# Kernel tuning notes

Hardware: AMD Instinct MI355X
Metric: run time of the kernel (lower is better)

## Reference

```python
import jax, jax.numpy as jnp
import numpy as np

B, C, L = 32, 512, 16          # batch, clauses per CNF, max literals per clause
D, H, P = 256, 1024, 16        # clause_hidden_dim, hidden_size, prefix_tokens
NH, NL = 8, 4                  # adapter_heads, adapter_layers
MAXV = 512                     # max_variables


def _ln(x, w, b, eps=1e-5):
    m = jnp.mean(x, axis=-1, keepdims=True)
    v = jnp.mean(jnp.square(x - m), axis=-1, keepdims=True)
    return (x - m) * jax.lax.rsqrt(v + eps) * w + b


def _mha(q, k, v, w_in, b_in, w_out, b_out, nh):
    E = q.shape[-1]
    dh = E // nh
    wq, wk, wv = jnp.split(w_in, 3, axis=0)
    bq, bk, bv = jnp.split(b_in, 3, axis=0)

    def heads(x, w, b):
        y = x @ w.T + b
        return y.reshape(x.shape[0], x.shape[1], nh, dh).transpose(0, 2, 1, 3)

    qh, kh, vh = heads(q, wq, bq), heads(k, wk, bk), heads(v, wv, bv)
    att = jax.nn.softmax(jnp.einsum('bhqd,bhkd->bhqk', qh, kh) * (1.0 / np.sqrt(dh)), axis=-1)
    o = jnp.einsum('bhqk,bhkd->bhqd', att, vh).transpose(0, 2, 1, 3).reshape(q.shape[0], q.shape[1], E)
    return o @ w_out.T + b_out


def setup_inputs() -> dict:
    key = jax.random.key(0)
    ks = jax.random.split(key, 16)
    s = 0.02
    var_idx = jax.random.randint(ks[0], (B, C, L), 0, MAXV + 1)
    sign_idx = jax.random.randint(ks[1], (B, C, L), 1, 3)   # 1=positive literal, 2=negative
    lens = jax.random.randint(ks[2], (B, C), 1, L + 1)      # ragged clause lengths >= 1
    lit_mask = jnp.arange(L)[None, None, :] < lens[..., None]
    inp = dict(var_idx=var_idx, sign_idx=sign_idx, lit_mask=lit_mask)
    inp['var_emb'] = jax.random.normal(ks[3], (MAXV + 1, D)) * s
    inp['sign_emb'] = jax.random.normal(ks[4], (3, D)) * s
    inp['litpos_emb'] = jax.random.normal(ks[5], (L, D)) * s
    inp['clausepos_emb'] = jax.random.normal(ks[6], (C, D)) * s
    inp['enc_in_w'] = jax.random.normal(ks[7], (NL, 3 * D, D)) * s
    inp['enc_in_b'] = jnp.zeros((NL, 3 * D))
    inp['enc_out_w'] = jax.random.normal(ks[8], (NL, D, D)) * s
    inp['enc_out_b'] = jnp.zeros((NL, D))
    inp['enc_ff1_w'] = jax.random.normal(ks[9], (NL, 4 * D, D)) * s
    inp['enc_ff1_b'] = jnp.zeros((NL, 4 * D))
    inp['enc_ff2_w'] = jax.random.normal(ks[10], (NL, D, 4 * D)) * s
    inp['enc_ff2_b'] = jnp.zeros((NL, D))
    inp['enc_n1_w'] = jnp.ones((NL, D))
    inp['enc_n1_b'] = jnp.zeros((NL, D))
    inp['enc_n2_w'] = jnp.ones((NL, D))
    inp['enc_n2_b'] = jnp.zeros((NL, D))
    inp['th_ln_w'] = jnp.ones((D,))
    inp['th_ln_b'] = jnp.zeros((D,))
    inp['th_w'] = jax.random.normal(ks[11], (H, D)) * s
    inp['th_b'] = jnp.zeros((H,))
    inp['pq'] = jax.random.normal(ks[12], (P, H))
    inp['pa_in_w'] = jax.random.normal(ks[13], (3 * H, H)) * s
    inp['pa_in_b'] = jnp.zeros((3 * H,))
    inp['pa_out_w'] = jax.random.normal(ks[14], (H, H)) * s
    inp['pa_out_b'] = jnp.zeros((H,))
    inp['pn_w'] = jnp.ones((H,))
    inp['pn_b'] = jnp.zeros((H,))
    return inp


def reference(var_idx, sign_idx, lit_mask, var_emb, sign_emb, litpos_emb, clausepos_emb,
              enc_in_w, enc_in_b, enc_out_w, enc_out_b, enc_ff1_w, enc_ff1_b,
              enc_ff2_w, enc_ff2_b, enc_n1_w, enc_n1_b, enc_n2_w, enc_n2_b,
              th_ln_w, th_ln_b, th_w, th_b, pq, pa_in_w, pa_in_b, pa_out_w, pa_out_b,
              pn_w, pn_b):
    # literal states [B,C,L,D]: four embedding gathers fused into one expression
    lit = (var_emb[var_idx] + sign_emb[sign_idx]
           + litpos_emb[None, None, :, :] + clausepos_emb[None, :, None, :])
    m = lit_mask[..., None].astype(lit.dtype)
    x = jnp.sum(lit * m, axis=2) / jnp.sum(m, axis=2)   # masked mean-pool -> [B,C,D]
    for i in range(NL):  # PyTorch post-norm TransformerEncoderLayer, gelu (exact)
        a = _mha(x, x, x, enc_in_w[i], enc_in_b[i], enc_out_w[i], enc_out_b[i], NH)
        x = _ln(x + a, enc_n1_w[i], enc_n1_b[i])
        f = jax.nn.gelu(x @ enc_ff1_w[i].T + enc_ff1_b[i], approximate=False) @ enc_ff2_w[i].T + enc_ff2_b[i]
        x = _ln(x + f, enc_n2_w[i], enc_n2_b[i])
    ch = _ln(x, th_ln_w, th_ln_b) @ th_w.T + th_b       # to_hidden -> [B,C,H]
    q = jnp.broadcast_to(pq[None], (ch.shape[0], P, H))
    pref = _mha(q, ch, ch, pa_in_w, pa_in_b, pa_out_w, pa_out_b, NH)
    return _ln(pref + q, pn_w, pn_b)                    # [B,P,H]
```

## Files before the change

kernel.cpp:

```cpp
#include <hip/hip_runtime.h>
#include <hip/hip_bf16.h>

typedef unsigned short u16;
typedef unsigned int u32;
typedef __attribute__((ext_vector_type(8))) short short8;
typedef __attribute__((ext_vector_type(4))) float floatx4;

#define BB 32
#define CC 512
#define LL 16
#define DD 256
#define HH 1024
#define PP 16
#define NLAY 4

__device__ __forceinline__ float bf2f(u16 u) {
  u32 x = ((u32)u) << 16; float f; __builtin_memcpy(&f, &x, 4); return f;
}
__device__ __forceinline__ u16 f2bf(float f) {
  __hip_bfloat16 h = __float2bfloat16(f);
  u16 r; __builtin_memcpy(&r, &h, 2); return r;
}
__device__ __forceinline__ void gload_lds16(const u16* g, u16* l) {
  __builtin_amdgcn_global_load_lds(
// ... 156 lines not shown
  }
  u32 cv = *(const u32*)&cpeb[c * DD + dl];
  float inv = 1.f / (float)cnt;
  u32 pk = (u32)f2bf(a0 * inv + bf2f((u16)cv)) | ((u32)f2bf(a1 * inv + bf2f((u16)(cv >> 16))) << 16);
  *(u32*)&xb[(size_t)bc * DD + dl] = pk;
}

template<int NC, bool GELU, bool LN, bool DLN>
__global__ __launch_bounds__(256) void gwide_kernel(
    const u16* __restrict__ A, const u16* __restrict__ W, const float* __restrict__ bias,
    const u16* __restrict__ resb, const float* __restrict__ gam, const float* __restrict__ bet,
    const float* __restrict__ gam2, const float* __restrict__ bet2,
    u16* __restrict__ out, int N, int K)
{
  constexpr int NT = NC / 32;
  constexpr int NT4 = NC / 64;
  __shared__ __align__(16) u16 As[32 * 64];
  __shared__ __align__(16) u16 Ws[NC * 64];
  __shared__ float sred[32][4][2];
  __shared__ float sred2[32][4][2];
  int t = threadIdx.x, lane = t & 63, w = t >> 6;
  int mrow = lane & 15, quad = lane >> 4;
  int bn0 = blockIdx.x * NC, bm0 = blockIdx.y * 32;

  int rA = t >> 3, gcA = (t & 7) ^ (rA & 7);
  const u16* gAp = A + (size_t)(bm0 + rA) * K + gcA * 8;
  u16* lAp = As + (w * 64) * 8;
  const u16* gW0 = W + (size_t)(bn0 + rA) * K + gcA * 8;
  u16* lW0 = Ws + (w * 64) * 8;

  floatx4 acc[2][NT4];
  #pragma unroll
  for (int mi = 0; mi < 2; ++mi)
    #pragma unroll
    for (int nt = 0; nt < NT4; ++nt) acc[mi][nt] = (floatx4){0.f, 0.f, 0.f, 0.f};

  for (int k0 = 0; k0 < K; k0 += 64) {
    __syncthreads();
    gload_lds16(gAp, lAp); gAp += 64;
    #pragma unroll
    for (int i = 0; i < NT; ++i)
      gload_lds16(gW0 + (size_t)i * 32 * K, lW0 + i * 2048);
    gW0 += 64;
    __syncthreads();
    #pragma unroll
    for (int ks = 0; ks < 2; ++ks) {
      int sw = ((ks * 4 + quad) ^ (mrow & 7)) * 8;
      short8 af0 = *(const short8*)&As[mrow * 64 + sw];
      short8 af1 = *(const short8*)&As[(16 + mrow) * 64 + sw];
      #pragma unroll
      for (int nt = 0; nt < NT4; ++nt) {
        int rw = w * (NC / 4) + nt * 16 + mrow;
        short8 bf = *(const short8*)&Ws[rw * 64 + sw];
        acc[0][nt] = __builtin_amdgcn_mfma_f32_16x16x32_bf16(af0, bf, acc[0][nt], 0, 0, 0);
        acc[1][nt] = __builtin_amdgcn_mfma_f32_16x16x32_bf16(af1, bf, acc[1][nt], 0, 0, 0);
      }
    }
  }

  if constexpr (LN) {
    float val[2][NT4][4];
    float bv[NT4];
    #pragma unroll
    for (int nt = 0; nt < NT4; ++nt) bv[nt] = bias[w * 64 + nt * 16 + mrow];
    #pragma unroll
    for (int mi = 0; mi < 2; ++mi) {
      #pragma unroll
      for (int r = 0; r < 4; ++r) {
        int gm = bm0 + mi * 16 + quad * 4 + r;
        float sr = 0.f, s2r = 0.f;
        #pragma unroll
        for (int nt = 0; nt < NT4; ++nt) {
          int gn = w * 64 + nt * 16 + mrow;
          float v = acc[mi][nt][r] + bv[nt] + bf2f(resb[(size_t)gm * 256 + gn]);
          val[mi][nt][r] = v; sr += v; s2r += v * v;
        }
        sr += __shfl_xor(sr, 1); s2r += __shfl_xor(s2r, 1);
        sr += __shfl_xor(sr, 2); s2r += __shfl_xor(s2r, 2);
        sr += __shfl_xor(sr, 4); s2r += __shfl_xor(s2r, 4);
        sr += __shfl_xor(sr, 8); s2r += __shfl_xor(s2r, 8);
        if (mrow == 0) { sred[mi * 16 + quad * 4 + r][w][0] = sr; sred[mi * 16 + quad * 4 + r][w][1] = s2r; }
      }
    }
    __syncthreads();
    #pragma unroll
    for (int mi = 0; mi < 2; ++mi) {
      #pragma unroll
      for (int r = 0; r < 4; ++r) {
        int lrow = mi * 16 + quad * 4 + r;
        float S  = sred[lrow][0][0] + sred[lrow][1][0] + sred[lrow][2][0] + sred[lrow][3][0];
        float S2 = sred[lrow][0][1] + sred[lrow][1][1] + sred[lrow][2][1] + sred[lrow][3][1];
        float mean = S * (1.f / 256.f);
        float var = S2 * (1.f / 256.f) - mean * mean;
        float inv = rsqrtf(var + 1e-5f);
        float sr2 = 0.f, s2r2 = 0.f;
        #pragma unroll
        for (int nt = 0; nt < NT4; ++nt) {
          int gn = w * 64 + nt * 16 + mrow;
          float y = (val[mi][nt][r] - mean) * inv * gam[gn] + bet[gn];
          val[mi][nt][r] = y;
          if constexpr (DLN) { sr2 += y; s2r2 += y * y; }
          else out[(size_t)(bm0 + lrow) * 256 + gn] = f2bf(y);
        }
        if constexpr (DLN) {
          sr2 += __shfl_xor(sr2, 1); s2r2 += __shfl_xor(s2r2, 1);
          sr2 += __shfl_xor(sr2, 2); s2r2 += __shfl_xor(s2r2, 2);
          sr2 += __shfl_xor(sr2, 4); s2r2 += __shfl_xor(s2r2, 4);
          sr2 += __shfl_xor(sr2, 8); s2r2 += __shfl_xor(s2r2, 8);
          if (mrow == 0) { sred2[lrow][w][0] = sr2; sred2[lrow][w][1] = s2r2; }
        }
      }
    }
    if constexpr (DLN) {
      __syncthreads();
      #pragma unroll
      for (int mi = 0; mi < 2; ++mi) {
        #pragma unroll
        for (int r = 0; r < 4; ++r) {
          int lrow = mi * 16 + quad * 4 + r;
          float S  = sred2[lrow][0][0] + sred2[lrow][1][0] + sred2[lrow][2][0] + sred2[lrow][3][0];
          float S2 = sred2[lrow][0][1] + sred2[lrow][1][1] + sred2[lrow][2][1] + sred2[lrow][3][1];
          float mean = S * (1.f / 256.f);
          float var = S2 * (1.f / 256.f) - mean * mean;
          float inv = rsqrtf(var + 1e-5f);
          #pragma unroll
          for (int nt = 0; nt < NT4; ++nt) {
            int gn = w * 64 + nt * 16 + mrow;
            float z = (val[mi][nt][r] - mean) * inv * gam2[gn] + bet2[gn];
            out[(size_t)(bm0 + lrow) * 256 + gn] = f2bf(z);
          }
        }
      }
    }
  } else {
    #pragma unroll
    for (int nt = 0; nt < NT4; ++nt) {
      int gn = bn0 + w * (NC / 4) + nt * 16 + mrow;
      float bv = bias[gn];
      #pragma unroll
      for (int mi = 0; mi < 2; ++mi) {
        #pragma unroll
        for (int r = 0; r < 4; ++r) {
          int gm = bm0 + mi * 16 + quad * 4 + r;
          float v = acc[mi][nt][r] + bv;
          if (GELU) v = 0.5f * v * (1.f + erff(v * 0.70710678118654752f));
          out[(size_t)gm * N + gn] = f2bf(v);
        }
      }
    }
  }
}

template<bool DLN>
__global__ __launch_bounds__(256) void ffu_kernel(
    const u16* __restrict__ A, const u16* __restrict__ W1, const float* __restrict__ b1,
    const u16* __restrict__ W2, const float* __restrict__ b2,
    const u16* __restrict__ resb,
    const float* __restrict__ gam, const float* __restrict__ bet,
    const float* __restrict__ gam2, const float* __restrict__ bet2,
    u16* __restrict__ out)
{
  __shared__ __align__(16) u16 As[2048];
  __shared__ __align__(16) u16 Ws[8 * 2048];
  __shared__ __align__(16) u16 Hs[4 * 2048];
  int t = threadIdx.x, lane = t & 63, w = t >> 6;
  int mrow = lane & 15, quad = lane >> 4;
  int bm0 = blockIdx.x * 32;
  int rA = t >> 3, gcA = (t & 7) ^ (rA & 7);

  floatx4 yacc[2][4];
  #pragma unroll
  for (int mi = 0; mi < 2; ++mi)
    #pragma unroll
    for (int nt = 0; nt < 4; ++nt) yacc[mi][nt] = (floatx4){0.f, 0.f, 0.f, 0.f};

  for (int nq = 0; nq < 4; ++nq) {
    floatx4 hacc[2][4];
    #pragma unroll
    for (int mi = 0; mi < 2; ++mi)
      #pragma unroll
      for (int nt = 0; nt < 4; ++nt) hacc[mi][nt] = (floatx4){0.f, 0.f, 0.f, 0.f};
    for (int kt = 0; kt < 4; ++kt) {
      __syncthreads();
      gload_lds16(A + (size_t)(bm0 + rA) * 256 + kt * 64 + gcA * 8, As + (w * 64) * 8);
      #pragma unroll
      for (int i = 0; i < 8; ++i)
        gload_lds16(W1 + (size_t)(nq * 256 + i * 32 + rA) * 256 + kt * 64 + gcA * 8,
                    Ws + i * 2048 + (w * 64) * 8);
      __syncthreads();
      #pragma unroll
      for (int ks = 0; ks < 2; ++ks) {
        int sw = ((ks * 4 + quad) ^ (mrow & 7)) * 8;
        short8 af0 = *(const short8*)&As[mrow * 64 + sw];
        short8 af1 = *(const short8*)&As[(16 + mrow) * 64 + sw];
        #pragma unroll
        for (int nt = 0; nt < 4; ++nt) {
          short8 bf = *(const short8*)&Ws[(w * 64 + nt * 16 + mrow) * 64 + sw];
          hacc[0][nt] = __builtin_amdgcn_mfma_f32_16x16x32_bf16(af0, bf, hacc[0][nt], 0, 0, 0);
          hacc[1][nt] = __builtin_amdgcn_mfma_f32_16x16x32_bf16(af1, bf, hacc[1][nt], 0, 0, 0);
        }
      }
    }
    {
      float bv1[4];
      #pragma unroll
      for (int nt = 0; nt < 4; ++nt) bv1[nt] = b1[nq * 256 + w * 64 + nt * 16 + mrow];
      #pragma unroll
      for (int mi = 0; mi < 2; ++mi) {
        #pragma unroll
        for (int nt = 0; nt < 4; ++nt) {
          int g = nt * 2 + (mrow >> 3);
          #pragma unroll
          for (int r = 0; r < 4; ++r) {
            int row = mi * 16 + quad * 4 + r;
            float v = hacc[mi][nt][r] + bv1[nt];
            v = 0.5f * v * (1.f + erff(v * 0.70710678118654752f));
            Hs[w * 2048 + row * 64 + (g ^ (row & 7)) * 8 + (mrow & 7)] = f2bf(v);
          }
        }
      }
    }
    for (int kt2 = 0; kt2 < 4; ++kt2) {
      __syncthreads();
      #pragma unroll
      for (int i = 0; i < 8; ++i)
        gload_lds16(W2 + (size_t)(i * 32 + rA) * 1024 + nq * 256 + kt2 * 64 + gcA * 8,
                    Ws + i * 2048 + (w * 64) * 8);
      __syncthreads();
      #pragma unroll
      for (int ks = 0; ks < 2; ++ks) {
        int sw = ((ks * 4 + quad) ^ (mrow & 7)) * 8;
        short8 af0 = *(const short8*)&Hs[kt2 * 2048 + mrow * 64 + sw];
        short8 af1 = *(const short8*)&Hs[kt2 * 2048 + (16 + mrow) * 64 + sw];
        #pragma unroll
        for (int nt = 0; nt < 4; ++nt) {
          short8 bf = *(const short8*)&Ws[(w * 64 + nt * 16 + mrow) * 64 + sw];
          yacc[0][nt] = __builtin_amdgcn_mfma_f32_16x16x32_bf16(af0, bf, yacc[0][nt], 0, 0, 0);
          yacc[1][nt] = __builtin_amdgcn_mfma_f32_16x16x32_bf16(af1, bf, yacc[1][nt], 0, 0, 0);
        }
      }
    }
  }
  __syncthreads();
  float* sred  = (float*)Hs;
  float* sred2 = (float*)(Hs + 2048);
  float val[2][4][4];
  float bv[4];
  #pragma unroll
  for (int nt = 0; nt < 4; ++nt) bv[nt] = b2[w * 64 + nt * 16 + mrow];
  #pragma unroll
  for (int mi = 0; mi < 2; ++mi) {
    #pragma unroll
    for (int r = 0; r < 4; ++r) {
      int gm = bm0 + mi * 16 + quad * 4 + r;
      float sr = 0.f, s2r = 0.f;
      #pragma unroll
      for (int nt = 0; nt < 4; ++nt) {
        int gn = w * 64 + nt * 16 + mrow;
        float v = yacc[mi][nt][r] + bv[nt] + bf2f(resb[(size_t)gm * 256 + gn]);
        val[mi][nt][r] = v; sr += v; s2r += v * v;
      }
      sr += __shfl_xor(sr, 1); s2r += __shfl_xor(s2r, 1);
      sr += __shfl_xor(sr, 2); s2r += __shfl_xor(s2r, 2);
      sr += __shfl_xor(sr, 4); s2r += __shfl_xor(s2r, 4);
      sr += __shfl_xor(sr, 8); s2r += __shfl_xor(s2r, 8);
      if (mrow == 0) {
        int lrow = mi * 16 + quad * 4 + r;
        sred[lrow * 8 + w * 2 + 0] = sr; sred[lrow * 8 + w * 2 + 1] = s2r;
      }
    }
  }
  __syncthreads();
  #pragma unroll
  for (int mi = 0; mi < 2; ++mi) {
    #pragma unroll
    for (int r = 0; r < 4; ++r) {
      int lrow = mi * 16 + quad * 4 + r;
      float S  = sred[lrow * 8 + 0] + sred[lrow * 8 + 2] + sred[lrow * 8 + 4] + sred[lrow * 8 + 6];
      float S2 = sred[lrow * 8 + 1] + sred[lrow * 8 + 3] + sred[lrow * 8 + 5] + sred[lrow * 8 + 7];
      float mean = S * (1.f / 256.f);
      float var = S2 * (1.f / 256.f) - mean * mean;
      float inv = rsqrtf(var + 1e-5f);
      float sr2 = 0.f, s2r2 = 0.f;
      #pragma unroll
      for (int nt = 0; nt < 4; ++nt) {
        int gn = w * 64 + nt * 16 + mrow;
        float y = (val[mi][nt][r] - mean) * inv * gam[gn] + bet[gn];
        val[mi][nt][r] = y;
        if constexpr (DLN) { sr2 += y; s2r2 += y * y; }
        else out[(size_t)(bm0 + lrow) * 256 + gn] = f2bf(y);
      }
      if constexpr (DLN) {
        sr2 += __shfl_xor(sr2, 1); s2r2 += __shfl_xor(s2r2, 1);
        sr2 += __shfl_xor(sr2, 2); s2r2 += __shfl_xor(s2r2, 2);
        sr2 += __shfl_xor(sr2, 4); s2r2 += __shfl_xor(s2r2, 4);
        sr2 += __shfl_xor(sr2, 8); s2r2 += __shfl_xor(s2r2, 8);
        if (mrow == 0) {
          sred2[lrow * 8 + w * 2 + 0] = sr2; sred2[lrow * 8 + w * 2 + 1] = s2r2;
        }
      }
    }
  }
  if constexpr (DLN) {
    __syncthreads();
    #pragma unroll
    for (int mi = 0; mi < 2; ++mi) {
      #pragma unroll
      for (int r = 0; r < 4; ++r) {
        int lrow = mi * 16 + quad * 4 + r;
        float S  = sred2[lrow * 8 + 0] + sred2[lrow * 8 + 2] + sred2[lrow * 8 + 4] + sred2[lrow * 8 + 6];
        float S2 = sred2[lrow * 8 + 1] + sred2[lrow * 8 + 3] + sred2[lrow * 8 + 5] + sred2[lrow * 8 + 7];
        float mean = S * (1.f / 256.f);
        float var = S2 * (1.f / 256.f) - mean * mean;
        float inv = rsqrtf(var + 1e-5f);
        #pragma unroll
        for (int nt = 0; nt < 4; ++nt) {
          int gn = w * 64 + nt * 16 + mrow;
          float z = (val[mi][nt][r] - mean) * inv * gam2[gn] + bet2[gn];
          out[(size_t)(bm0 + lrow) * 256 + gn] = f2bf(z);
        }
      }
    }
  }
}

__global__ __launch_bounds__(256) void gemm128_kernel(
    const u16* __restrict__ A, const u16* __restrict__ W, const float* __restrict__ bias,
    const float* __restrict__ res, void* __restrict__ out,
    int M, int N, int K, int flags)
{
  __shared__ __align__(16) u16 As[128 * 64];
  __shared__ __align__(16) u16 Bs[128 * 64];
  int t = threadIdx.x;
  int lane = t & 63, w = t >> 6;
  int wm = w & 1, wn = w >> 1;
  int bn0 = blockIdx.x * 128, bm0 = blockIdx.y * 128;
  int mrow = lane & 15, quad = lane >> 4;
  int z = blockIdx.z, NZ = gridDim.z;
  int Kc = K / NZ, kbase = z * Kc;

  const u16* gA[4]; const u16* gB[4];
  u16* lA[4]; u16* lB[4];
  #pragma unroll
  for (int it = 0; it < 4; ++it) {
    int c = w * 256 + it * 64 + lane;
    int r = c >> 3;
    int gc = (c & 7) ^ (r & 7);
    gA[it] = A + (size_t)(bm0 + r) * K + kbase + gc * 8;
    gB[it] = W + (size_t)(bn0 + r) * K + kbase + gc * 8;
    lA[it] = As + (w * 256 + it * 64) * 8;
    lB[it] = Bs + (w * 256 + it * 64) * 8;
  }
  floatx4 acc[4][4];
  #pragma unroll
  for (int i = 0; i < 4; ++i)
    #pragma unroll
    for (int j = 0; j < 4; ++j)
      acc[i][j] = (floatx4){0.f, 0.f, 0.f, 0.f};
  int sw0 = ((0 * 4 + quad) ^ (mrow & 7)) * 8;
  int sw1 = ((1 * 4 + quad) ^ (mrow & 7)) * 8;

  for (int k0 = 0; k0 < Kc; k0 += 64) {
    __syncthreads();
    #pragma unroll
    for (int it = 0; it < 4; ++it) { gload_lds16(gA[it], lA[it]); gA[it] += 64; }
    #pragma unroll
    for (int it = 0; it < 4; ++it) { gload_lds16(gB[it], lB[it]); gB[it] += 64; }
    __syncthreads();
    #pragma unroll
    for (int ks = 0; ks < 2; ++ks) {
      int sw = ks ? sw1 : sw0;
      short8 af[4], bfr[4];
      #pragma unroll
      for (int mi = 0; mi < 4; ++mi)
        af[mi] = *(const short8*)&As[(wm * 64 + mi * 16 + mrow) * 64 + sw];
      #pragma unroll
      for (int nj = 0; nj < 4; ++nj)
        bfr[nj] = *(const short8*)&Bs[(wn * 64 + nj * 16 + mrow) * 64 + sw];
      #pragma unroll
      for (int mi = 0; mi < 4; ++mi)
        #pragma unroll
        for (int nj = 0; nj < 4; ++nj)
          acc[mi][nj] = __builtin_amdgcn_mfma_f32_16x16x32_bf16(af[mi], bfr[nj], acc[mi][nj], 0, 0, 0);
    }
  }
  if (NZ > 1) {
    float* po = (float*)out + (size_t)z * M * N;
    #pragma unroll
    for (int nj = 0; nj < 4; ++nj) {
      int gn = bn0 + wn * 64 + nj * 16 + mrow;
      #pragma unroll
      for (int mi = 0; mi < 4; ++mi)
        #pragma unroll
        for (int r = 0; r < 4; ++r) {
          int gm = bm0 + wm * 64 + mi * 16 + quad * 4 + r;
          po[(size_t)gm * N + gn] = acc[mi][nj][r];
        }
    }
    return;
  }
  bool do_gelu = (flags & 1) != 0, of32 = (flags & 2) != 0;
  #pragma unroll
  for (int nj = 0; nj < 4; ++nj) {
    int gn = bn0 + wn * 64 + nj * 16 + mrow;
    float bv = bias ? bias[gn] : 0.f;
    #pragma unroll
    for (int mi = 0; mi < 4; ++mi) {
      #pragma unroll
      for (int r = 0; r < 4; ++r) {
        int gm = bm0 + wm * 64 + mi * 16 + quad * 4 + r;
        float v = acc[mi][nj][r] + bv;
        if (do_gelu) v = 0.5f * v * (1.f + erff(v * 0.70710678118654752f));
        if (flags & 4) v += res[(size_t)(gm & 15) * N + gn];
        else if (res) v += res[(size_t)gm * N + gn];
        if (of32) ((float*)out)[(size_t)gm * N + gn] = v;
        else      ((u16*)out)[(size_t)gm * N + gn] = f2bf(v);
      }
    }
  }
}

template<int D>
__global__ __launch_bounds__(256) void lnw_kernel(
    const float* __restrict__ in, const float* __restrict__ w, const float* __restrict__ b,
    float* __restrict__ outf, u16* __restrict__ outb)
{
  constexpr int NV = D / 64;
  int lane = threadIdx.x & 63, wv = threadIdx.x >> 6;
  int row = blockIdx.x * 4 + wv;
  const float* xr = in + (size_t)row * D;
  float v[NV];
  float s = 0.f, s2 = 0.f;
  #pragma unroll
  for (int i = 0; i < NV; ++i) {
    v[i] = xr[lane + i * 64];
    s += v[i]; s2 += v[i] * v[i];
  }
  #pragma unroll
  for (int off = 32; off > 0; off >>= 1) { s += __shfl_xor(s, off); s2 += __shfl_xor(s2, off); }
  float mean = s / (float)D;
  float var = s2 / (float)D - mean * mean;
  float inv = rsqrtf(var + 1e-5f);
  #pragma unroll
  for (int i = 0; i < NV; ++i) {
    int col = lane + i * 64;
    float y = (v[i] - mean) * inv * w[col] + b[col];
    size_t o = (size_t)row * D + col;
    if (outf) outf[o] = y;
    if (outb) outb[o] = f2bf(y);
  }
}

__global__ __launch_bounds__(256, 5) void attn_enc6_kernel(
    const u16* __restrict__ qkv, u16* __restrict__ out)
{
  __shared__ __align__(16) u16 Ks[64 * 40];
  __shared__ __align__(16) u16 Vt[32 * 72];
  __shared__ __align__(16) u16 Pl[4 * 32 * 72];
  int F = blockIdx.x;
  int xcd = F & 7, jj = F >> 3;
  int pair = xcd * 32 + (jj >> 2), qt = jj & 3;
  int b = pair >> 3, h = pair & 7;
  int t = threadIdx.x, lane = t & 63, w = t >> 6;
  int mrow = lane & 15, quad = lane >> 4;
  int q0 = qt * 128 + w * 32;
  short8 qf[2];
  #pragma unroll
  for (int mi = 0; mi < 2; ++mi)
    qf[mi] = *(const short8*)(qkv + (size_t)(b * CC + q0 + mi * 16 + mrow) * 768 + h * 32 + quad * 8);
  floatx4 o[2][2];
  #pragma unroll
  for (int mi = 0; mi < 2; ++mi)
// ... 81 lines not shown
  const float sc = 0.08838834764831845f * 1.4426950408889634f;
  const floatx4 zf = (floatx4){0.f, 0.f, 0.f, 0.f};
  {
    int q = t >> 4, c0 = (t & 15) * 16;
    *(uint4*)&Qs[q * 264 + c0]     = *(const uint4*)(qcg + ((size_t)h * 16 + q) * 256 + c0);
    *(uint4*)&Qs[q * 264 + c0 + 8] = *(const uint4*)(qcg + ((size_t)h * 16 + q) * 256 + c0 + 8);
  }
  floatx4 Tacc[4] = {zf, zf, zf, zf};
  float lacc = 0.f;
  const u16* tb = tln + (size_t)b * 512 * 256;
  for (int jt = 0; jt < 8; ++jt) {
    __syncthreads();
    {
      int j = t >> 2, c0 = (t & 3) * 64;
      #pragma unroll
      for (int u = 0; u < 8; ++u) {
        uint4 v = *(const uint4*)(tb + (size_t)(jt * 64 + j) * 256 + c0 + u * 8);
        *(uint4*)&Ajc[j * 264 + c0 + u * 8] = v;
        u16 tmp[8]; *(uint4*)tmp = v;
        #pragma unroll
        for (int i = 0; i < 8; ++i) Acj[(c0 + u * 8 + i) * 72 + j] = tmp[i];
      }
    }
    __syncthreads();
    floatx4 s = zf;
    #pragma unroll
    for (int kk = 0; kk < 8; ++kk) {
      short8 af = *(const short8*)&Ajc[(w * 16 + mrow) * 264 + kk * 32 + quad * 8];
      short8 bf = *(const short8*)&Qs[mrow * 264 + kk * 32 + quad * 8];
      s = __builtin_amdgcn_mfma_f32_16x16x32_bf16(af, bf, s, 0, 0, 0);
    }
    u16 hv[4]; float ps = 0.f;
    #pragma unroll
    for (int r = 0; r < 4; ++r) {
      float p = exp2f(s[r] * sc);
      ps += p; hv[r] = f2bf(p);
    }
    ps += __shfl_xor(ps, 16); ps += __shfl_xor(ps, 32);
    lacc += ps;
    *(uint2*)&Ps[mrow * 72 + w * 16 + quad * 4] = *(uint2*)hv;
    __syncthreads();
    #pragma unroll
    for (int kk = 0; kk < 2; ++kk) {
      short8 af = *(const short8*)&Ps[mrow * 72 + kk * 32 + quad * 8];
      #pragma unroll
      for (int ct = 0; ct < 4; ++ct) {
        short8 bf = *(const short8*)&Acj[(w * 64 + ct * 16 + mrow) * 72 + kk * 32 + quad * 8];
        Tacc[ct] = __builtin_amdgcn_mfma_f32_16x16x32_bf16(af, bf, Tacc[ct], 0, 0, 0);
      }
    }
  }
  if (lane < 16) Lred[w][lane] = lacc;
  __syncthreads();
  #pragma unroll
  for (int r = 0; r < 4; ++r) {
    int q = quad * 4 + r;
    float l = Lred[0][q] + Lred[1][q] + Lred[2][q] + Lred[3][q];
    float inv = 1.f / l;
    #pragma unroll
    for (int ct = 0; ct < 4; ++ct)
      Ts[q * 264 + w * 64 + ct * 16 + mrow] = f2bf(Tacc[ct][r] * inv);
  }
  __syncthreads();
  const u16* wv = wcb + (size_t)(1024 + h * 128) * 256;
  floatx4 oacc[2] = {zf, zf};
  #pragma unroll
  for (int kk = 0; kk < 8; ++kk) {
    short8 af = *(const short8*)&Ts[mrow * 264 + kk * 32 + quad * 8];
    #pragma unroll
    for (int dt = 0; dt < 2; ++dt) {
      short8 bf = *(const short8*)(wv + (size_t)(w * 32 + dt * 16 + mrow) * 256 + kk * 32 + quad * 8);
      oacc[dt] = __builtin_amdgcn_mfma_f32_16x16x32_bf16(af, bf, oacc[dt], 0, 0, 0);
    }
  }
  #pragma unroll
  for (int dt = 0; dt < 2; ++dt) {
    int d = w * 32 + dt * 16 + mrow;
    float bv = bkv[1024 + h * 128 + d];
    #pragma unroll
    for (int r = 0; r < 4; ++r) {
      int q = quad * 4 + r;
      out[((size_t)(b * 16 + q)) * 1024 + h * 128 + d] = f2bf(oacc[dt][r] + bv);
    }
  }
}

extern "C" void kernel_launch(void* const* d_in, const int* in_sizes, int n_in,
                              void* d_out, int out_size, void* d_ws, size_t ws_size,
                              hipStream_t stream)
{
  const int* vi = (const int*)d_in[0];
  const int* si = (const int*)d_in[1];
  const int* mk = (const int*)d_in[2];
  const float* ve   = (const float*)d_in[3];
  const float* se   = (const float*)d_in[4];
  const float* lpe  = (const float*)d_in[5];
  const float* cpe  = (const float*)d_in[6];
  const float* eiw  = (const float*)d_in[7];
  const float* eib  = (const float*)d_in[8];
  const float* eow  = (const float*)d_in[9];
  const float* eob  = (const float*)d_in[10];
  const float* f1w  = (const float*)d_in[11];
  const float* f1b  = (const float*)d_in[12];
  const float* f2w  = (const float*)d_in[13];
  const float* f2b  = (const float*)d_in[14];
  const float* n1w  = (const float*)d_in[15];
  const float* n1b  = (const float*)d_in[16];
  const float* n2w  = (const float*)d_in[17];
  const float* n2b  = (const float*)d_in[18];
  const float* tlw  = (const float*)d_in[19];
  const float* tlb  = (const float*)d_in[20];
  const float* thw  = (const float*)d_in[21];
  const float* thb  = (const float*)d_in[22];
  const float* pq   = (const float*)d_in[23];
  const float* paiw = (const float*)d_in[24];
  const float* paib = (const float*)d_in[25];
  const float* paow = (const float*)d_in[26];
  const float* paob = (const float*)d_in[27];
  const float* pnw  = (const float*)d_in[28];
  const float* pnb  = (const float*)d_in[29];

  const int NROW = BB * CC;
  const size_t MB = 1048576;
  char* base = (char*)d_ws;
  u16* xb   = (u16*)(base);
  u16* qkvb = (u16*)(base + 8 * MB);
  u16* atto = (u16*)(base + 32 * MB);
  u16* tln  = (u16*)(base + 96 * MB);
  u16* wcb   = (u16*)(base + 64 * MB);
  u16* thwTb = (u16*)(base + 65 * MB);
  float* bkv = (float*)(base + 66 * MB);
  u16* wckT  = (u16*)(base + 67 * MB);
  u16* qcg   = (u16*)(base + 68 * MB);
  float* skpart = (float*)(base + 80 * MB);
  u16* wbf  = (u16*)(base + 104 * MB);
  u16* qh    = (u16*)(base + 120 * MB);
  u16* prefo = (u16*)(base + 121 * MB);
  float* prefout = (float*)(base + 122 * MB);

  u16* eiw_b  = wbf + 0;
  u16* eow_b  = wbf + 786432;
  u16* f1w_b  = wbf + 1048576;
  u16* f2w_b  = wbf + 2097152;
  u16* thw_b  = wbf + 3145728;
  u16* paiw_b = wbf + 3407872;
  u16* paow_b = wbf + 6553600;
  u16* pqb    = wbf + 7602176;
  u16* veb    = wbf + 7618560;
  u16* seb    = wbf + 7749888;
  u16* lpeb   = wbf + 7750656;
  u16* cpeb   = wbf + 7754752;

  dim3 blk(256);
  cvt_kernel<<<7701, blk, 0, stream>>>(eiw, eow, f1w, f2w, thw, paiw, paow, pq,
                                       ve, se, lpe, cpe, wbf);
  thwT_kernel<<<256, blk, 0, stream>>>(thw, thwTb);
  biasfold_kernel<<<512, blk, 0, stream>>>(paiw_b + (size_t)HH * HH, thb, paib, bkv);
  gemm128_kernel<<<dim3(2, 16, 4), blk, 0, stream>>>(
      paiw_b + (size_t)HH * HH, thwTb, nullptr, nullptr, skpart, 2048, 256, HH, 0);
  redk_kernel<<<512, blk, 0, stream>>>(skpart, nullptr, nullptr, nullptr, wcb,
                                       256, 4, 2048 * 256, 0);
  gemm128_kernel<<<dim3(8, 1, 8), blk, 0, stream>>>(
      pqb, paiw_b, nullptr, nullptr, skpart, 128, 1024, HH, 0);
  redk_kernel<<<128, blk, 0, stream>>>(skpart, paib, nullptr, nullptr, qh,
                                       1024, 8, 128 * 1024, 0);
  bT_kernel<<<256, blk, 0, stream>>>(wcb, wckT);
  qc_kernel<<<8, blk, 0, stream>>>(qh, wckT, qcg);
  embed_kernel<<<NROW/2, blk, 0, stream>>>(vi, si, mk, veb, seb, lpeb, cpeb, xb);
  for (int i = 0; i < NLAY; ++i) {
    gwide_kernel<384, false, false, false><<<dim3(2, NROW/32), blk, 0, stream>>>(
        xb, eiw_b + (size_t)i*768*DD, eib + i*768, nullptr, nullptr, nullptr, nullptr, nullptr,
        qkvb, 768, DD);
    attn_enc6_kernel<<<1024, blk, 0, stream>>>(qkvb, atto);
    gwide_kernel<256, false, true, false><<<dim3(1, NROW/32), blk, 0, stream>>>(
        atto, eow_b + (size_t)i*DD*DD, eob + i*DD, xb, n1w + i*DD, n1b + i*DD, nullptr, nullptr,
        xb, DD, DD);
    if (i < NLAY - 1) {
      ffu_kernel<false><<<NROW/32, blk, 0, stream>>>(
          xb, f1w_b + (size_t)i*HH*DD, f1b + i*HH, f2w_b + (size_t)i*DD*HH, f2b + i*DD,
          xb, n2w + i*DD, n2b + i*DD, nullptr, nullptr, xb);
    } else {
      ffu_kernel<true><<<NROW/32, blk, 0, stream>>>(
          xb, f1w_b + (size_t)i*HH*DD, f1b + i*HH, f2w_b + (size_t)i*DD*HH, f2b + i*DD,
          xb, n2w + i*DD, n2b + i*DD, tlw, tlb, tln);
    }
  }
  attn_preff_kernel<<<dim3(BB, 8), blk, 0, stream>>>(tln, wcb, qcg, bkv, prefo);
  gemm128_kernel<<<dim3(1024/128, (BB*PP)/128, 4), blk, 0, stream>>>(
      prefo, paow_b, nullptr, nullptr, skpart, BB*PP, HH, HH, 0);
  redk_kernel<<<512, blk, 0, stream>>>(skpart, paob, pq, prefout, nullptr,
                                       1024, 4, BB*PP*HH, 4);
  lnw_kernel<1024><<<(BB*PP)/4, blk, 0, stream>>>(prefout, pnw, pnb, (float*)d_out, nullptr);
}
```

Before: 659.1 us.

## Double FFN row tile to 64 with 2x2 warp layout and resident X tile

The fused FFN kernel now handles 64 rows per block instead of 32. It arranges the 4 waves as 2 row halves by 2 column halves, each computing a 32x128 sub-tile. The full 64x256 input tile is loaded once into shared memory up front, so it is no longer reloaded for every hidden quarter. Each streamed W1/W2 tile is reused across twice as many rows, halving weight traffic per row. The cost is doubled accumulator registers (hacc and yacc 2x8 each), larger shared memory (~96KB), and half as many blocks (256), which may lower occupancy and latency hiding.

```diff
diff --git a/kernel.cpp b/kernel.cpp
--- a/kernel.cpp
+++ b/kernel.cpp
@@ -340,29 +340,40 @@
     const float* __restrict__ gam2, const float* __restrict__ bet2,
     u16* __restrict__ out)
 {
-  __shared__ __align__(16) u16 As[2048];
+  __shared__ __align__(16) u16 Xs[4 * 4096];
   __shared__ __align__(16) u16 Ws[8 * 2048];
-  __shared__ __align__(16) u16 Hs[4 * 2048];
+  __shared__ __align__(16) u16 Hs[4 * 4096];
   int t = threadIdx.x, lane = t & 63, w = t >> 6;
   int mrow = lane & 15, quad = lane >> 4;
-  int bm0 = blockIdx.x * 32;
+  int rh = w & 1, ch = w >> 1;
+  int bm0 = blockIdx.x * 64;
   int rA = t >> 3, gcA = (t & 7) ^ (rA & 7);
 
-  floatx4 yacc[2][4];
+  #pragma unroll
+  for (int kt = 0; kt < 4; ++kt) {
+    #pragma unroll
+    for (int i = 0; i < 2; ++i) {
+      int idx = i * 256 + t;
+      int r = idx >> 3, gc = (idx & 7) ^ (r & 7);
+      gload_lds16(A + (size_t)(bm0 + r) * 256 + kt * 64 + gc * 8,
+                  Xs + kt * 4096 + (i * 256 + w * 64) * 8);
+    }
+  }
+
+  floatx4 yacc[2][8];
   #pragma unroll
   for (int mi = 0; mi < 2; ++mi)
     #pragma unroll
-    for (int nt = 0; nt < 4; ++nt) yacc[mi][nt] = (floatx4){0.f, 0.f, 0.f, 0.f};
+    for (int nt = 0; nt < 8; ++nt) yacc[mi][nt] = (floatx4){0.f, 0.f, 0.f, 0.f};
 
   for (int nq = 0; nq < 4; ++nq) {
-    floatx4 hacc[2][4];
+    floatx4 hacc[2][8];
     #pragma unroll
     for (int mi = 0; mi < 2; ++mi)
       #pragma unroll
-      for (int nt = 0; nt < 4; ++nt) hacc[mi][nt] = (floatx4){0.f, 0.f, 0.f, 0.f};
+      for (int nt = 0; nt < 8; ++nt) hacc[mi][nt] = (floatx4){0.f, 0.f, 0.f, 0.f};
     for (int kt = 0; kt < 4; ++kt) {
       __syncthreads();
-      gload_lds16(A + (size_t)(bm0 + rA) * 256 + kt * 64 + gcA * 8, As + (w * 64) * 8);
       #pragma unroll
       for (int i = 0; i < 8; ++i)
         gload_lds16(W1 + (size_t)(nq * 256 + i * 32 + rA) * 256 + kt * 64 + gcA * 8,
@@ -371,31 +382,32 @@
       #pragma unroll
       for (int ks = 0; ks < 2; ++ks) {
         int sw = ((ks * 4 + quad) ^ (mrow & 7)) * 8;
-        short8 af0 = *(const short8*)&As[mrow * 64 + sw];
-        short8 af1 = *(const short8*)&As[(16 + mrow) * 64 + sw];
-        #pragma unroll
-        for (int nt = 0; nt < 4; ++nt) {
-          short8 bf = *(const short8*)&Ws[(w * 64 + nt * 16 + mrow) * 64 + sw];
+        short8 af0 = *(const short8*)&Xs[kt * 4096 + (rh * 32 + mrow) * 64 + sw];
+        short8 af1 = *(const short8*)&Xs[kt * 4096 + (rh * 32 + 16 + mrow) * 64 + sw];
+        #pragma unroll
+        for (int nt = 0; nt < 8; ++nt) {
+          short8 bf = *(const short8*)&Ws[(ch * 128 + nt * 16 + mrow) * 64 + sw];
           hacc[0][nt] = __builtin_amdgcn_mfma_f32_16x16x32_bf16(af0, bf, hacc[0][nt], 0, 0, 0);
           hacc[1][nt] = __builtin_amdgcn_mfma_f32_16x16x32_bf16(af1, bf, hacc[1][nt], 0, 0, 0);
         }
       }
     }
     {
-      float bv1[4];
-      #pragma unroll
-      for (int nt = 0; nt < 4; ++nt) bv1[nt] = b1[nq * 256 + w * 64 + nt * 16 + mrow];
+      float bv1[8];
+      #pragma unroll
+      for (int nt = 0; nt < 8; ++nt) bv1[nt] = b1[nq * 256 + ch * 128 + nt * 16 + mrow];
       #pragma unroll
       for (int mi = 0; mi < 2; ++mi) {
         #pragma unroll
-        for (int nt = 0; nt < 4; ++nt) {
-          int g = nt * 2 + (mrow >> 3);
+        for (int nt = 0; nt < 8; ++nt) {
+          int kt2 = ch * 2 + (nt >> 2);
+          int g = (nt & 3) * 2 + (mrow >> 3);
           #pragma unroll
           for (int r = 0; r < 4; ++r) {
-            int row = mi * 16 + quad * 4 + r;
+            int row = rh * 32 + mi * 16 + quad * 4 + r;
             float v = hacc[mi][nt][r] + bv1[nt];
             v = 0.5f * v * (1.f + erff(v * 0.70710678118654752f));
-            Hs[w * 2048 + row * 64 + (g ^ (row & 7)) * 8 + (mrow & 7)] = f2bf(v);
+            Hs[kt2 * 4096 + row * 64 + (g ^ (row & 7)) * 8 + (mrow & 7)] = f2bf(v);
           }
         }
       }
@@ -410,11 +422,11 @@
       #pragma unroll
       for (int ks = 0; ks < 2; ++ks) {
         int sw = ((ks * 4 + quad) ^ (mrow & 7)) * 8;
-        short8 af0 = *(const short8*)&Hs[kt2 * 2048 + mrow * 64 + sw];
-        short8 af1 = *(const short8*)&Hs[kt2 * 2048 + (16 + mrow) * 64 + sw];
-        #pragma unroll
-        for (int nt = 0; nt < 4; ++nt) {
-          short8 bf = *(const short8*)&Ws[(w * 64 + nt * 16 + mrow) * 64 + sw];
+        short8 af0 = *(const short8*)&Hs[kt2 * 4096 + (rh * 32 + mrow) * 64 + sw];
+        short8 af1 = *(const short8*)&Hs[kt2 * 4096 + (rh * 32 + 16 + mrow) * 64 + sw];
+        #pragma unroll
+        for (int nt = 0; nt < 8; ++nt) {
+          short8 bf = *(const short8*)&Ws[(ch * 128 + nt * 16 + mrow) * 64 + sw];
           yacc[0][nt] = __builtin_amdgcn_mfma_f32_16x16x32_bf16(af0, bf, yacc[0][nt], 0, 0, 0);
           yacc[1][nt] = __builtin_amdgcn_mfma_f32_16x16x32_bf16(af1, bf, yacc[1][nt], 0, 0, 0);
         }
@@ -422,21 +434,22 @@
     }
   }
   __syncthreads();
-  float* sred  = (float*)Hs;
-  float* sred2 = (float*)(Hs + 2048);
-  float val[2][4][4];
-  float bv[4];
-  #pragma unroll
-  for (int nt = 0; nt < 4; ++nt) bv[nt] = b2[w * 64 + nt * 16 + mrow];
+  float* sred  = (float*)Xs;
+  float* sred2 = sred + 256;
+  float val[2][8][4];
+  float bv[8];
+  #pragma unroll
+  for (int nt = 0; nt < 8; ++nt) bv[nt] = b2[ch * 128 + nt * 16 + mrow];
   #pragma unroll
   for (int mi = 0; mi < 2; ++mi) {
     #pragma unroll
     for (int r = 0; r < 4; ++r) {
-      int gm = bm0 + mi * 16 + quad * 4 + r;
+      int row = rh * 32 + mi * 16 + quad * 4 + r;
+      int gm = bm0 + row;
       float sr = 0.f, s2r = 0.f;
       #pragma unroll
-      for (int nt = 0; nt < 4; ++nt) {
-        int gn = w * 64 + nt * 16 + mrow;
+      for (int nt = 0; nt < 8; ++nt) {
+        int gn = ch * 128 + nt * 16 + mrow;
         float v = yacc[mi][nt][r] + bv[nt] + bf2f(resb[(size_t)gm * 256 + gn]);
         val[mi][nt][r] = v; sr += v; s2r += v * v;
       }
@@ -444,10 +457,7 @@
       sr += __shfl_xor(sr, 2); s2r += __shfl_xor(s2r, 2);
       sr += __shfl_xor(sr, 4); s2r += __shfl_xor(s2r, 4);
       sr += __shfl_xor(sr, 8); s2r += __shfl_xor(s2r, 8);
-      if (mrow == 0) {
-        int lrow = mi * 16 + quad * 4 + r;
-        sred[lrow * 8 + w * 2 + 0] = sr; sred[lrow * 8 + w * 2 + 1] = s2r;
-      }
+      if (mrow == 0) { sred[row * 4 + ch * 2 + 0] = sr; sred[row * 4 + ch * 2 + 1] = s2r; }
     }
   }
   __syncthreads();
@@ -455,29 +465,27 @@
   for (int mi = 0; mi < 2; ++mi) {
     #pragma unroll
     for (int r = 0; r < 4; ++r) {
-      int lrow = mi * 16 + quad * 4 + r;
-      float S  = sred[lrow * 8 + 0] + sred[lrow * 8 + 2] + sred[lrow * 8 + 4] + sred[lrow * 8 + 6];
-      float S2 = sred[lrow * 8 + 1] + sred[lrow * 8 + 3] + sred[lrow * 8 + 5] + sred[lrow * 8 + 7];
+      int row = rh * 32 + mi * 16 + quad * 4 + r;
+      float S  = sred[row * 4 + 0] + sred[row * 4 + 2];
+      float S2 = sred[row * 4 + 1] + sred[row * 4 + 3];
       float mean = S * (1.f / 256.f);
       float var = S2 * (1.f / 256.f) - mean * mean;
       float inv = rsqrtf(var + 1e-5f);
       float sr2 = 0.f, s2r2 = 0.f;
       #pragma unroll
-      for (int nt = 0; nt < 4; ++nt) {
-        int gn = w * 64 + nt * 16 + mrow;
+      for (int nt = 0; nt < 8; ++nt) {
+        int gn = ch * 128 + nt * 16 + mrow;
         float y = (val[mi][nt][r] - mean) * inv * gam[gn] + bet[gn];
         val[mi][nt][r] = y;
         if constexpr (DLN) { sr2 += y; s2r2 += y * y; }
-        else out[(size_t)(bm0 + lrow) * 256 + gn] = f2bf(y);
+        else out[(size_t)(bm0 + row) * 256 + gn] = f2bf(y);
       }
       if constexpr (DLN) {
         sr2 += __shfl_xor(sr2, 1); s2r2 += __shfl_xor(s2r2, 1);
         sr2 += __shfl_xor(sr2, 2); s2r2 += __shfl_xor(s2r2, 2);
         sr2 += __shfl_xor(sr2, 4); s2r2 += __shfl_xor(s2r2, 4);
         sr2 += __shfl_xor(sr2, 8); s2r2 += __shfl_xor(s2r2, 8);
-        if (mrow == 0) {
-          sred2[lrow * 8 + w * 2 + 0] = sr2; sred2[lrow * 8 + w * 2 + 1] = s2r2;
-        }
+        if (mrow == 0) { sred2[row * 4 + ch * 2 + 0] = sr2; sred2[row * 4 + ch * 2 + 1] = s2r2; }
       }
     }
   }
@@ -487,17 +495,17 @@
     for (int mi = 0; mi < 2; ++mi) {
       #pragma unroll
       for (int r = 0; r < 4; ++r) {
-        int lrow = mi * 16 + quad * 4 + r;
-        float S  = sred2[lrow * 8 + 0] + sred2[lrow * 8 + 2] + sred2[lrow * 8 + 4] + sred2[lrow * 8 + 6];
-        float S2 = sred2[lrow * 8 + 1] + sred2[lrow * 8 + 3] + sred2[lrow * 8 + 5] + sred2[lrow * 8 + 7];
+        int row = rh * 32 + mi * 16 + quad * 4 + r;
+        float S  = sred2[row * 4 + 0] + sred2[row * 4 + 2];
+        float S2 = sred2[row * 4 + 1] + sred2[row * 4 + 3];
         float mean = S * (1.f / 256.f);
         float var = S2 * (1.f / 256.f) - mean * mean;
         float inv = rsqrtf(var + 1e-5f);
         #pragma unroll
-        for (int nt = 0; nt < 4; ++nt) {
-          int gn = w * 64 + nt * 16 + mrow;
+        for (int nt = 0; nt < 8; ++nt) {
+          int gn = ch * 128 + nt * 16 + mrow;
           float z = (val[mi][nt][r] - mean) * inv * gam2[gn] + bet2[gn];
-          out[(size_t)(bm0 + lrow) * 256 + gn] = f2bf(z);
+          out[(size_t)(bm0 + row) * 256 + gn] = f2bf(z);
         }
       }
     }
@@ -909,11 +917,11 @@
         atto, eow_b + (size_t)i*DD*DD, eob + i*DD, xb, n1w + i*DD, n1b + i*DD, nullptr, nullptr,
         xb, DD, DD);
     if (i < NLAY - 1) {
-      ffu_kernel<false><<<NROW/32, blk, 0, stream>>>(
+      ffu_kernel<false><<<NROW/64, blk, 0, stream>>>(
           xb, f1w_b + (size_t)i*HH*DD, f1b + i*HH, f2w_b + (size_t)i*DD*HH, f2b + i*DD,
           xb, n2w + i*DD, n2b + i*DD, nullptr, nullptr, xb);
     } else {
-      ffu_kernel<true><<<NROW/32, blk, 0, stream>>>(
+      ffu_kernel<true><<<NROW/64, blk, 0, stream>>>(
           xb, f1w_b + (size_t)i*HH*DD, f1b + i*HH, f2w_b + (size_t)i*DD*HH, f2b + i*DD,
           xb, n2w + i*DD, n2b + i*DD, tlw, tlb, tln);
     }
```

After: 847.6 us. 28.6% more time.

## Double FFN row tile to 64 with 512-thread blocks sharing weight tiles

Applied to the files above, without the earlier changes.

The fused FFN kernel now processes 64 rows per block with 8 waves (two row halves by four column groups) instead of 32 rows with 4 waves. Each W1/W2 tile loaded into LDS is reused across twice as many rows, halving the total weight traffic per layer. LDS use grows (the hidden buffer doubles), and the grid halves to NROW/64 blocks, which may reduce occupancy and load balance across CUs. The reduction scratch moves into the A buffer to avoid clobbering the hidden buffer.

```diff
diff --git a/kernel.cpp b/kernel.cpp
--- a/kernel.cpp
+++ b/kernel.cpp
@@ -332,7 +332,7 @@
 }
 
 template<bool DLN>
-__global__ __launch_bounds__(256) void ffu_kernel(
+__global__ __launch_bounds__(512) void ffu_kernel(
     const u16* __restrict__ A, const u16* __restrict__ W1, const float* __restrict__ b1,
     const u16* __restrict__ W2, const float* __restrict__ b2,
     const u16* __restrict__ resb,
@@ -340,12 +340,13 @@
     const float* __restrict__ gam2, const float* __restrict__ bet2,
     u16* __restrict__ out)
 {
-  __shared__ __align__(16) u16 As[2048];
-  __shared__ __align__(16) u16 Ws[8 * 2048];
-  __shared__ __align__(16) u16 Hs[4 * 2048];
+  __shared__ __align__(16) u16 As[4096];
+  __shared__ __align__(16) u16 Ws[16384];
+  __shared__ __align__(16) u16 Hs[4 * 4096];
   int t = threadIdx.x, lane = t & 63, w = t >> 6;
   int mrow = lane & 15, quad = lane >> 4;
-  int bm0 = blockIdx.x * 32;
+  int rh = w >> 2, wc = w & 3;
+  int bm0 = blockIdx.x * 64;
   int rA = t >> 3, gcA = (t & 7) ^ (rA & 7);
 
   floatx4 yacc[2][4];
@@ -364,18 +365,18 @@
       __syncthreads();
       gload_lds16(A + (size_t)(bm0 + rA) * 256 + kt * 64 + gcA * 8, As + (w * 64) * 8);
       #pragma unroll
-      for (int i = 0; i < 8; ++i)
-        gload_lds16(W1 + (size_t)(nq * 256 + i * 32 + rA) * 256 + kt * 64 + gcA * 8,
-                    Ws + i * 2048 + (w * 64) * 8);
+      for (int i = 0; i < 4; ++i)
+        gload_lds16(W1 + (size_t)(nq * 256 + i * 64 + rA) * 256 + kt * 64 + gcA * 8,
+                    Ws + i * 4096 + (w * 64) * 8);
       __syncthreads();
       #pragma unroll
       for (int ks = 0; ks < 2; ++ks) {
         int sw = ((ks * 4 + quad) ^ (mrow & 7)) * 8;
-        short8 af0 = *(const short8*)&As[mrow * 64 + sw];
-        short8 af1 = *(const short8*)&As[(16 + mrow) * 64 + sw];
+        short8 af0 = *(const short8*)&As[(rh * 32 + mrow) * 64 + sw];
+        short8 af1 = *(const short8*)&As[(rh * 32 + 16 + mrow) * 64 + sw];
         #pragma unroll
         for (int nt = 0; nt < 4; ++nt) {
-          short8 bf = *(const short8*)&Ws[(w * 64 + nt * 16 + mrow) * 64 + sw];
+          short8 bf = *(const short8*)&Ws[(wc * 64 + nt * 16 + mrow) * 64 + sw];
           hacc[0][nt] = __builtin_amdgcn_mfma_f32_16x16x32_bf16(af0, bf, hacc[0][nt], 0, 0, 0);
           hacc[1][nt] = __builtin_amdgcn_mfma_f32_16x16x32_bf16(af1, bf, hacc[1][nt], 0, 0, 0);
         }
@@ -384,7 +385,7 @@
     {
       float bv1[4];
       #pragma unroll
-      for (int nt = 0; nt < 4; ++nt) bv1[nt] = b1[nq * 256 + w * 64 + nt * 16 + mrow];
+      for (int nt = 0; nt < 4; ++nt) bv1[nt] = b1[nq * 256 + wc * 64 + nt * 16 + mrow];
       #pragma unroll
       for (int mi = 0; mi < 2; ++mi) {
         #pragma unroll
@@ -392,10 +393,10 @@
           int g = nt * 2 + (mrow >> 3);
           #pragma unroll
           for (int r = 0; r < 4; ++r) {
-            int row = mi * 16 + quad * 4 + r;
+            int row = rh * 32 + mi * 16 + quad * 4 + r;
             float v = hacc[mi][nt][r] + bv1[nt];
             v = 0.5f * v * (1.f + erff(v * 0.70710678118654752f));
-            Hs[w * 2048 + row * 64 + (g ^ (row & 7)) * 8 + (mrow & 7)] = f2bf(v);
+            Hs[wc * 4096 + row * 64 + (g ^ (row & 7)) * 8 + (mrow & 7)] = f2bf(v);
           }
         }
       }
@@ -403,18 +404,18 @@
     for (int kt2 = 0; kt2 < 4; ++kt2) {
       __syncthreads();
       #pragma unroll
-      for (int i = 0; i < 8; ++i)
-        gload_lds16(W2 + (size_t)(i * 32 + rA) * 1024 + nq * 256 + kt2 * 64 + gcA * 8,
-                    Ws + i * 2048 + (w * 64) * 8);
+      for (int i = 0; i < 4; ++i)
+        gload_lds16(W2 + (size_t)(i * 64 + rA) * 1024 + nq * 256 + kt2 * 64 + gcA * 8,
+                    Ws + i * 4096 + (w * 64) * 8);
       __syncthreads();
       #pragma unroll
       for (int ks = 0; ks < 2; ++ks) {
         int sw = ((ks * 4 + quad) ^ (mrow & 7)) * 8;
-        short8 af0 = *(const short8*)&Hs[kt2 * 2048 + mrow * 64 + sw];
-        short8 af1 = *(const short8*)&Hs[kt2 * 2048 + (16 + mrow) * 64 + sw];
+        short8 af0 = *(const short8*)&Hs[kt2 * 4096 + (rh * 32 + mrow) * 64 + sw];
+        short8 af1 = *(const short8*)&Hs[kt2 * 4096 + (rh * 32 + 16 + mrow) * 64 + sw];
         #pragma unroll
         for (int nt = 0; nt < 4; ++nt) {
-          short8 bf = *(const short8*)&Ws[(w * 64 + nt * 16 + mrow) * 64 + sw];
+          short8 bf = *(const short8*)&Ws[(wc * 64 + nt * 16 + mrow) * 64 + sw];
           yacc[0][nt] = __builtin_amdgcn_mfma_f32_16x16x32_bf16(af0, bf, yacc[0][nt], 0, 0, 0);
           yacc[1][nt] = __builtin_amdgcn_mfma_f32_16x16x32_bf16(af1, bf, yacc[1][nt], 0, 0, 0);
         }
@@ -422,21 +423,22 @@
     }
   }
   __syncthreads();
-  float* sred  = (float*)Hs;
-  float* sred2 = (float*)(Hs + 2048);
+  float* sred  = (float*)As;
+  float* sred2 = sred + 512;
   float val[2][4][4];
   float bv[4];
   #pragma unroll
-  for (int nt = 0; nt < 4; ++nt) bv[nt] = b2[w * 64 + nt * 16 + mrow];
+  for (int nt = 0; nt < 4; ++nt) bv[nt] = b2[wc * 64 + nt * 16 + mrow];
   #pragma unroll
   for (int mi = 0; mi < 2; ++mi) {
     #pragma unroll
     for (int r = 0; r < 4; ++r) {
-      int gm = bm0 + mi * 16 + quad * 4 + r;
+      int row = rh * 32 + mi * 16 + quad * 4 + r;
+      int gm = bm0 + row;
       float sr = 0.f, s2r = 0.f;
       #pragma unroll
       for (int nt = 0; nt < 4; ++nt) {
-        int gn = w * 64 + nt * 16 + mrow;
+        int gn = wc * 64 + nt * 16 + mrow;
         float v = yacc[mi][nt][r] + bv[nt] + bf2f(resb[(size_t)gm * 256 + gn]);
         val[mi][nt][r] = v; sr += v; s2r += v * v;
       }
@@ -444,10 +446,7 @@
       sr += __shfl_xor(sr, 2); s2r += __shfl_xor(s2r, 2);
       sr += __shfl_xor(sr, 4); s2r += __shfl_xor(s2r, 4);
       sr += __shfl_xor(sr, 8); s2r += __shfl_xor(s2r, 8);
-      if (mrow == 0) {
-        int lrow = mi * 16 + quad * 4 + r;
-        sred[lrow * 8 + w * 2 + 0] = sr; sred[lrow * 8 + w * 2 + 1] = s2r;
-      }
+      if (mrow == 0) { sred[row * 8 + wc * 2 + 0] = sr; sred[row * 8 + wc * 2 + 1] = s2r; }
     }
   }
   __syncthreads();
@@ -455,29 +454,27 @@
   for (int mi = 0; mi < 2; ++mi) {
     #pragma unroll
     for (int r = 0; r < 4; ++r) {
-      int lrow = mi * 16 + quad * 4 + r;
-      float S  = sred[lrow * 8 + 0] + sred[lrow * 8 + 2] + sred[lrow * 8 + 4] + sred[lrow * 8 + 6];
-      float S2 = sred[lrow * 8 + 1] + sred[lrow * 8 + 3] + sred[lrow * 8 + 5] + sred[lrow * 8 + 7];
+      int row = rh * 32 + mi * 16 + quad * 4 + r;
+      float S  = sred[row * 8 + 0] + sred[row * 8 + 2] + sred[row * 8 + 4] + sred[row * 8 + 6];
+      float S2 = sred[row * 8 + 1] + sred[row * 8 + 3] + sred[row * 8 + 5] + sred[row * 8 + 7];
       float mean = S * (1.f / 256.f);
       float var = S2 * (1.f / 256.f) - mean * mean;
       float inv = rsqrtf(var + 1e-5f);
       float sr2 = 0.f, s2r2 = 0.f;
       #pragma unroll
       for (int nt = 0; nt < 4; ++nt) {
-        int gn = w * 64 + nt * 16 + mrow;
+        int gn = wc * 64 + nt * 16 + mrow;
         float y = (val[mi][nt][r] - mean) * inv * gam[gn] + bet[gn];
         val[mi][nt][r] = y;
         if constexpr (DLN) { sr2 += y; s2r2 += y * y; }
-        else out[(size_t)(bm0 + lrow) * 256 + gn] = f2bf(y);
+        else out[(size_t)(bm0 + row) * 256 + gn] = f2bf(y);
       }
       if constexpr (DLN) {
         sr2 += __shfl_xor(sr2, 1); s2r2 += __shfl_xor(s2r2, 1);
         sr2 += __shfl_xor(sr2, 2); s2r2 += __shfl_xor(s2r2, 2);
         sr2 += __shfl_xor(sr2, 4); s2r2 += __shfl_xor(s2r2, 4);
         sr2 += __shfl_xor(sr2, 8); s2r2 += __shfl_xor(s2r2, 8);
-        if (mrow == 0) {
-          sred2[lrow * 8 + w * 2 + 0] = sr2; sred2[lrow * 8 + w * 2 + 1] = s2r2;
-        }
+        if (mrow == 0) { sred2[row * 8 + wc * 2 + 0] = sr2; sred2[row * 8 + wc * 2 + 1] = s2r2; }
       }
     }
   }
@@ -487,17 +484,17 @@
     for (int mi = 0; mi < 2; ++mi) {
       #pragma unroll
       for (int r = 0; r < 4; ++r) {
-        int lrow = mi * 16 + quad * 4 + r;
-        float S  = sred2[lrow * 8 + 0] + sred2[lrow * 8 + 2] + sred2[lrow * 8 + 4] + sred2[lrow * 8 + 6];
-        float S2 = sred2[lrow * 8 + 1] + sred2[lrow * 8 + 3] + sred2[lrow * 8 + 5] + sred2[lrow * 8 + 7];
+        int row = rh * 32 + mi * 16 + quad * 4 + r;
+        float S  = sred2[row * 8 + 0] + sred2[row * 8 + 2] + sred2[row * 8 + 4] + sred2[row * 8 + 6];
+        float S2 = sred2[row * 8 + 1] + sred2[row * 8 + 3] + sred2[row * 8 + 5] + sred2[row * 8 + 7];
         float mean = S * (1.f / 256.f);
         float var = S2 * (1.f / 256.f) - mean * mean;
         float inv = rsqrtf(var + 1e-5f);
         #pragma unroll
         for (int nt = 0; nt < 4; ++nt) {
-          int gn = w * 64 + nt * 16 + mrow;
+          int gn = wc * 64 + nt * 16 + mrow;
           float z = (val[mi][nt][r] - mean) * inv * gam2[gn] + bet2[gn];
-          out[(size_t)(bm0 + lrow) * 256 + gn] = f2bf(z);
+          out[(size_t)(bm0 + row) * 256 + gn] = f2bf(z);
         }
       }
     }
@@ -885,6 +882,7 @@
   u16* cpeb   = wbf + 7754752;
 
   dim3 blk(256);
+  dim3 blk512(512);
   cvt_kernel<<<7701, blk, 0, stream>>>(eiw, eow, f1w, f2w, thw, paiw, paow, pq,
                                        ve, se, lpe, cpe, wbf);
   thwT_kernel<<<256, blk, 0, stream>>>(thw, thwTb);
@@ -909,11 +907,11 @@
         atto, eow_b + (size_t)i*DD*DD, eob + i*DD, xb, n1w + i*DD, n1b + i*DD, nullptr, nullptr,
         xb, DD, DD);
     if (i < NLAY - 1) {
-      ffu_kernel<false><<<NROW/32, blk, 0, stream>>>(
+      ffu_kernel<false><<<NROW/64, blk512, 0, stream>>>(
           xb, f1w_b + (size_t)i*HH*DD, f1b + i*HH, f2w_b + (size_t)i*DD*HH, f2b + i*DD,
           xb, n2w + i*DD, n2b + i*DD, nullptr, nullptr, xb);
     } else {
-      ffu_kernel<true><<<NROW/32, blk, 0, stream>>>(
+      ffu_kernel<true><<<NROW/64, blk512, 0, stream>>>(
           xb, f1w_b + (size_t)i*HH*DD, f1b + i*HH, f2w_b + (size_t)i*DD*HH, f2b + i*DD,
           xb, n2w + i*DD, n2b + i*DD, tlw, tlb, tln);
     }
```

New measurement: 655.4 us. Within noise of the previous version (-0.6%).
